# Kernel tuning notes

Hardware: AMD Instinct MI355X
Metric: run time of the kernel (lower is better)

Reference implementation:

```python
import jax, jax.numpy as jnp
import numpy as np
from jax import lax

PERM_AD = np.array([3, 0, 1, 6, 4, 2, 7, 8, 5])  # angular-difference kernel permutation
IDX_HD_POS = np.array([0, 3, 6]); IDX_HD_NEG = np.array([2, 5, 8])
IDX_VD_POS = np.array([0, 1, 2]); IDX_VD_NEG = np.array([6, 7, 8])
TOP_K = 1
THETA = 1.0


def conv2d_3x3(x, w, b):
    # x: [B,C,H,W], w: [O,I,3,3], b: [O]; stride 1, padding 1
    out = lax.conv_general_dilated(x, w, window_strides=(1, 1), padding=((1, 1), (1, 1)),
                                   dimension_numbers=('NCHW', 'OIHW', 'NCHW'))
    return out + b[None, :, None, None]


def setup_inputs() -> dict:
    key = jax.random.key(0)
    ks = jax.random.split(key, 12)
    B, C, H, W, E = 16, 64, 128, 128, 5

    def winit(k, shape, fan_in):
        return jax.random.normal(k, shape, jnp.float32) * (1.0 / np.sqrt(fan_in))

    return {
        'x': jax.random.normal(ks[0], (B, C, H, W), jnp.float32),
        'noise': jax.random.normal(ks[1], (B, E), jnp.float32),
        'w_gate': winit(ks[2], (C, E), C), 'b_gate': jnp.zeros((E,), jnp.float32),
        'w_noise': winit(ks[3], (C, E), C), 'b_noise': jnp.zeros((E,), jnp.float32),
        'w1': winit(ks[4], (C, C, 3, 3), C * 9), 'b1': jnp.zeros((C,), jnp.float32),
        'w_cd': winit(ks[5], (C, C, 3, 3), C * 9), 'b_cd': jnp.zeros((C,), jnp.float32),
        'w_hd': winit(ks[6], (C, C, 3), C * 3), 'b_hd': jnp.zeros((C,), jnp.float32),
        'w_vd': winit(ks[7], (C, C, 3), C * 3), 'b_vd': jnp.zeros((C,), jnp.float32),
        'w_ad': winit(ks[8], (C, C, 3, 3), C * 9), 'b_ad': jnp.zeros((C,), jnp.float32),
    }


def reference(x, noise, w_gate, b_gate, w_noise, b_noise,
              w1, b1, w_cd, b_cd, w_hd, b_hd, w_vd, b_vd, w_ad, b_ad):
    B, C, H, W = x.shape
    E = w_gate.shape[1]

    # ---- NoisyTopkRouter on globally pooled features ----
    pooled = x.mean(axis=(2, 3))                      # [B, C]
    logits = pooled @ w_gate + b_gate                 # [B, E]
    noise_logits = pooled @ w_noise + b_noise         # [B, E]
    noisy = logits + noise * jax.nn.softplus(noise_logits)
    topv, topi = lax.top_k(noisy, TOP_K)              # [B, k]
    sparse = jnp.full_like(noisy, -jnp.inf)
    sparse = sparse.at[jnp.arange(B)[:, None], topi].set(topv)
    gates = jax.nn.softmax(sparse, axis=-1)           # [B, E]; 0 for unselected, gate weight otherwise

    # ---- Difference-convolution expert kernels ----
    wcd_f = w_cd.reshape(C, C, 9)
    wcd = wcd_f.at[:, :, 4].add(-wcd_f.sum(-1)).reshape(C, C, 3, 3)   # center = w4 - sum(all)
    whd = jnp.zeros((C, C, 9), x.dtype).at[:, :, IDX_HD_POS].set(w_hd).at[:, :, IDX_HD_NEG].set(-w_hd).reshape(C, C, 3, 3)
    wvd = jnp.zeros((C, C, 9), x.dtype).at[:, :, IDX_VD_POS].set(w_vd).at[:, :, IDX_VD_NEG].set(-w_vd).reshape(C, C, 3, 3)
    wad_f = w_ad.reshape(C, C, 9)
    wad = (wad_f - THETA * wad_f[:, :, PERM_AD]).reshape(C, C, 3, 3)

    outs = jnp.stack([
        conv2d_3x3(x, w1, b1),
        conv2d_3x3(x, wcd, b_cd),
        conv2d_3x3(x, whd, b_hd),
        conv2d_3x3(x, wvd, b_vd),
        conv2d_3x3(x, wad, b_ad),
    ], axis=0)                                        # [E, B, C, H, W]

    # ---- SparseDispatcher.combine: per-example softmax over flattened depth, gate-weighted scatter-add ----
    flat = outs.reshape(E, B, C * H * W)
    sm = jax.nn.softmax(flat, axis=-1)                # softmax over depth dim, as in combine()
    combined = jnp.einsum('ebd,be->bd', sm, gates)    # gates are 0 for non-dispatched (expert,example) pairs
    return combined.reshape(B, C, H, W)
```

## Files before the change

### kernel.cpp

```cpp
#include <hip/hip_runtime.h>
#include <math.h>

#define B_  16
#define C_  64
#define E_  5

typedef __bf16  bf16x8 __attribute__((ext_vector_type(8)));
typedef float   f32x4  __attribute__((ext_vector_type(4)));

#define WS_WEFFB   0
#define WS_BIAS    368640
#define WS_POOL    369920
#define WS_Z       374016
#define WS_CNT     374080
#define WS_XT      376128
#define WS_EXP     33930560ull
#define WS_NEED_A  67484992ull

static __device__ __forceinline__ unsigned short f2bf(float f) {
    unsigned int u = __float_as_uint(f);
    unsigned int r = (u + 0x7fffu + ((u >> 16) & 1u)) >> 16;
    return (unsigned short)r;
}

__global__ __launch_bounds__(256) void transpose_build_kernel(
        const float* __restrict__ x, unsigned short* __restrict__ x_t,
        float* __restrict__ pooled,
        const float* __restrict__ w1, const float* __restrict__ w_cd,
        const float* __restrict__ w_hd, const float* __restrict__ w_vd,
        const float* __restrict__ w_ad,
        const float* __restrict__ b1, const float* __restrict__ b_cd,
        const float* __restrict__ b_hd, const float* __restrict__ b_vd,
        const float* __restrict__ b_ad,
        unsigned short* __restrict__ wEffB, float* __restrict__ biasEff) {
    int bid = blockIdx.x;
    int t = threadIdx.x;

    if (bid >= 2048) {
        int gid = (bid - 2048) * 256 + t;
        if (gid < E_ * 36864) {
            int e   = gid / 36864;
            int r   = gid % 36864;
            int g   = r / 18432;
            int r2  = r % 18432;
            int tap = r2 / 2048;
            int r3  = r2 % 2048;
            int q   = r3 / 512;
            int r4  = r3 % 512;
            int co  = r4 / 8;
            int j   = r4 % 8;
            int ci = g * 32 + q * 8 + j;
            int base9 = (co * 64 + ci) * 9;
            int base3 = (co * 64 + ci) * 3;
            float v = 0.f;
            if (e == 0) {
                v = w1[base9 + tap];
            } else if (e == 1) {
                if (tap == 4) {
                    float s = 0.f;
                    #pragma unroll
                    for (int k = 0; k < 9; k++) s += w_cd[base9 + k];
                    v = w_cd[base9 + 4] - s;
                } else {
                    v = w_cd[base9 + tap];
                }
            } else if (e == 2) {
                int m = tap % 3;
                if (m == 0) v = w_hd[base3 + tap / 3];
                else if (m == 2) v = -w_hd[base3 + tap / 3];
            } else if (e == 3) {
                if (tap < 3) v = w_vd[base3 + tap];
                else if (tap >= 6) v = -w_vd[base3 + tap - 6];
            } else {
                const int PERM[9] = {3, 0, 1, 6, 4, 2, 7, 8, 5};
                v = w_ad[base9 + tap] - w_ad[base9 + PERM[tap]];
            }
            wEffB[gid] = f2bf(v);
        } else if (gid < E_ * 36864 + E_ * 64) {
            int jj = gid - E_ * 36864;
            int e = jj / 64, co = jj % 64;
            const float* bs;
            switch (e) {
                case 0: bs = b1; break;
                case 1: bs = b_cd; break;
                case 2: bs = b_hd; break;
                case 3: bs = b_vd; break;
                default: bs = b_ad; break;
            }
            biasEff[jj] = bs[co];
        }
        return;
    }

    int b = bid >> 7, row = bid & 127;
    int wave = t >> 6, l = t & 63;
    int half = l >> 5;
    int c4 = l & 31;

    __shared__ unsigned short T[128][72];

    const float* xb = x + (size_t)b * (64 * 16384) + row * 128;

    #pragma unroll
    for (int it = 0; it < 8; it++) {
        int ci = wave * 16 + it * 2 + half;
        float4 v = *(const float4*)(xb + (size_t)ci * 16384 + c4 * 4);
        float p = v.x + v.y + v.z + v.w;
        p += __shfl_down(p, 16, 32);
        p += __shfl_down(p, 8, 32);
        p += __shfl_down(p, 4, 32);
        p += __shfl_down(p, 2, 32);
        p += __shfl_down(p, 1, 32);
        if (c4 == 0) atomicAdd(&pooled[b * 64 + ci], p * (1.0f / 16384.0f));
        int colb = c4 * 4;
        T[colb + 0][ci] = f2bf(v.x);
        T[colb + 1][ci] = f2bf(v.y);
        T[colb + 2][ci] = f2bf(v.z);
        T[colb + 3][ci] = f2bf(v.w);
    }
    __syncthreads();

    unsigned short* dst = x_t + ((size_t)(b * 128 + row) * 128) * 64;
    #pragma unroll
    for (int k = 0; k < 4; k++) {
        int chunk = t + k * 256;
        int col = chunk >> 3, c8 = chunk & 7;
        uint4 vv = *(const uint4*)&T[col][c8 * 8];
        *(uint4*)(dst + col * 64 + c8 * 8) = vv;
    }
}

__global__ __launch_bounds__(256, 4) void conv_mfma_kernel(
        const unsigned short* __restrict__ x_t, const unsigned short* __restrict__ wEffB,
        const float* __restrict__ biasEff,
        const float* __restrict__ pooled, const float* __restrict__ noise,
        const float* __restrict__ w_gate, const float* __restrict__ b_gate,
        const float* __restrict__ w_noise, const float* __restrict__ b_noise,
        unsigned short* __restrict__ expw, float* __restrict__ outf,
        float* __restrict__ Z, int direct_f32) {
    int bid = blockIdx.x;
    int b = bid >> 6;
    int rem = bid & 63;
    int rg = rem >> 1;
    int ch = rem & 1;

    int t = threadIdx.x;
    int wave = t >> 6;
    int lane = t & 63;
    int ln = lane & 15;
    int q = lane >> 4;

    __shared__ __align__(16) unsigned short A_lds[3 * 4 * 66 * 8];
    __shared__ __align__(16) unsigned short Xs[4 * 4 * 68 * 8];
    __shared__ float zs[4];
    __shared__ int   se_sh;

    if (wave == 0) {
        float pv = pooled[b * C_ + lane];
        float ge[E_], ne[E_];
        #pragma unroll
        for (int e = 0; e < E_; e++) {
            ge[e] = pv * w_gate[lane * E_ + e];
            ne[e] = pv * w_noise[lane * E_ + e];
        }
        #pragma unroll
        for (int off = 32; off; off >>= 1) {
            #pragma unroll
            for (int e = 0; e < E_; e++) {
                ge[e] += __shfl_xor(ge[e], off, 64);
                ne[e] += __shfl_xor(ne[e], off, 64);
            }
        }
        if (lane == 0) {
            float best = -1e30f; int bi = 0;
            #pragma unroll
            for (int e = 0; e < E_; e++) {
                float lg = ge[e] + b_gate[e];
                float nz = ne[e] + b_noise[e];
                float sp = log1pf(expf(nz));
                float v = lg + noise[b * E_ + e] * sp;
                if (v > best) { best = v; bi = e; }
            }
            se_sh = bi;
        }
    }
    __syncthreads();
    int e = se_sh;

    f32x4 acc[4][4];
    #pragma unroll
    for (int i = 0; i < 4; i++)
        #pragma unroll
        for (int jn = 0; jn < 4; jn++)
            acc[i][jn] = (f32x4){0.f, 0.f, 0.f, 0.f};

    const unsigned short* xb = x_t + (size_t)b * (128 * 128 * 64);
    const unsigned short* we = wEffB + (size_t)e * 36864;

    for (int g = 0; g < 2; g++) {
        const uint4* asrc = (const uint4*)(we + g * 18432);
        #pragma unroll
        for (int chunk = 0; chunk < 3; chunk++) {
            if (chunk == 0) {
                for (int j = t; j < 1056; j += 256) {
                    int xr = j / 264;
                    int r2 = j % 264;
                    int col = r2 >> 2;
                    int qq = r2 & 3;
                    int irow = rg * 4 - 1 + xr;
                    int icol = ch * 64 - 1 + col;
                    uint4 v = make_uint4(0, 0, 0, 0);
                    if ((unsigned)irow < 128u && (unsigned)icol < 128u)
                        v = *(const uint4*)(xb + ((size_t)irow * 128 + icol) * 64 + g * 32 + qq * 8);
                    *(uint4*)&Xs[(((xr & 3) * 4 + qq) * 68 + col) * 8] = v;
                }
            } else {
                int xr = 3 + chunk;
                int irow = rg * 4 - 1 + xr;
                for (int j = t; j < 264; j += 256) {
                    int col = j >> 2;
                    int qq = j & 3;
                    int icol = ch * 64 - 1 + col;
                    uint4 v = make_uint4(0, 0, 0, 0);
                    if ((unsigned)irow < 128u && (unsigned)icol < 128u)
                        v = *(const uint4*)(xb + ((size_t)irow * 128 + icol) * 64 + g * 32 + qq * 8);
                    *(uint4*)&Xs[(((xr & 3) * 4 + qq) * 68 + col) * 8] = v;
                }
            }
            #pragma unroll
            for (int k = 0; k < 3; k++) {
                int j = t + k * 256;
                int slotrow = j >> 6;
                int m = j & 63;
                *(uint4*)&A_lds[(slotrow * 66 + m) * 8] = asrc[chunk * 768 + j];
            }
            __syncthreads();

            int xrl = wave + chunk;
            #pragma unroll
            for (int tl = 0; tl < 3; tl++) {
                bf16x8 af[4], bfr[4];
                #pragma unroll
                for (int mt = 0; mt < 4; mt++)
                    af[mt] = *(const bf16x8*)&A_lds[((tl * 4 + q) * 66 + mt * 16 + ln) * 8];
                #pragma unroll
                for (int t4 = 0; t4 < 4; t4++)
                    bfr[t4] = *(const bf16x8*)&Xs[(((xrl & 3) * 4 + q) * 68 + t4 * 16 + ln + tl) * 8];
                #pragma unroll
                for (int mt = 0; mt < 4; mt++)
                    #pragma unroll
                    for (int t4 = 0; t4 < 4; t4++)
                        acc[mt][t4] = __builtin_amdgcn_mfma_f32_16x16x32_bf16(
                            af[mt], bfr[t4], acc[mt][t4], 0, 0, 0);
            }
            __syncthreads();
        }
    }

    int orow = rg * 4 + wave;
    float bsum = 0.f;
    size_t obase = (size_t)b * (64 * 16384);
    #pragma unroll
    for (int mt = 0; mt < 4; mt++) {
        float4 bias4 = *(const float4*)(biasEff + e * 64 + mt * 16 + q * 4);
        const float* bp = (const float*)&bias4;
        #pragma unroll
        for (int r = 0; r < 4; r++) {
            int co = mt * 16 + q * 4 + r;
            size_t cb = obase + (size_t)co * 16384 + (size_t)orow * 128;
            #pragma unroll
            for (int t4 = 0; t4 < 4; t4++) {
                float ev = __expf(acc[mt][t4][r] + bp[r]);
                bsum += ev;
                int ocol = ch * 64 + t4 * 16 + ln;
                if (direct_f32) outf[cb + ocol] = ev;
                else            expw[cb + ocol] = f2bf(ev);
            }
        }
    }
    for (int off = 32; off; off >>= 1) bsum += __shfl_down(bsum, off, 64);
    if (lane == 0) zs[wave] = bsum;
    __syncthreads();
    if (t == 0) atomicAdd(&Z[b], zs[0] + zs[1] + zs[2] + zs[3]);
}

#define N_UINT4 2097152
__global__ __launch_bounds__(256) void scale_bf16_kernel(
        const unsigned short* __restrict__ expw, const float* __restrict__ Z,
        float* __restrict__ out) {
    __shared__ float sinv[B_];
    if (threadIdx.x < B_) sinv[threadIdx.x] = 1.0f / Z[threadIdx.x];
    __syncthreads();
    for (int gid = blockIdx.x * 256 + threadIdx.x; gid < N_UINT4; gid += 2048 * 256) {
        int b = gid >> 17;
        float s = sinv[b];
        uint4 r = ((const uint4*)expw)[gid];
        f32x4 o0, o1;
        o0[0] = __uint_as_float(r.x << 16) * s;
        o0[1] = __uint_as_float(r.x & 0xffff0000u) * s;
        o0[2] = __uint_as_float(r.y << 16) * s;
        o0[3] = __uint_as_float(r.y & 0xffff0000u) * s;
        o1[0] = __uint_as_float(r.z << 16) * s;
        o1[1] = __uint_as_float(r.z & 0xffff0000u) * s;
        o1[2] = __uint_as_float(r.w << 16) * s;
        o1[3] = __uint_as_float(r.w & 0xffff0000u) * s;
        __builtin_nontemporal_store(o0, &((f32x4*)out)[gid * 2]);
        __builtin_nontemporal_store(o1, &((f32x4*)out)[gid * 2 + 1]);
    }
}

#define N_FLOAT4 4194304
__global__ __launch_bounds__(256) void scale_inplace_kernel(
        float* __restrict__ out, const float* __restrict__ Z) {
    __shared__ float sinv[B_];
    if (threadIdx.x < B_) sinv[threadIdx.x] = 1.0f / Z[threadIdx.x];
    __syncthreads();
    for (int gid = blockIdx.x * 256 + threadIdx.x; gid < N_FLOAT4; gid += 2048 * 256) {
        int b = gid >> 18;
        float s = sinv[b];
        float4 v = ((float4*)out)[gid];
        v.x *= s; v.y *= s; v.z *= s; v.w *= s;
        ((float4*)out)[gid] = v;
    }
}

extern "C" void kernel_launch(void* const* d_in, const int* in_sizes, int n_in,
                              void* d_out, int out_size, void* d_ws, size_t ws_size,
                              hipStream_t stream) {
    const float* x       = (const float*)d_in[0];
    const float* noise   = (const float*)d_in[1];
    const float* w_gate  = (const float*)d_in[2];
    const float* b_gate  = (const float*)d_in[3];
    const float* w_noise = (const float*)d_in[4];
    const float* b_noise = (const float*)d_in[5];
    const float* w1      = (const float*)d_in[6];
    const float* b1      = (const float*)d_in[7];
    const float* w_cd    = (const float*)d_in[8];
    const float* b_cd    = (const float*)d_in[9];
    const float* w_hd    = (const float*)d_in[10];
    const float* b_hd    = (const float*)d_in[11];
    const float* w_vd    = (const float*)d_in[12];
    const float* b_vd    = (const float*)d_in[13];
    const float* w_ad    = (const float*)d_in[14];
    const float* b_ad    = (const float*)d_in[15];

    char* ws = (char*)d_ws;
    unsigned short* wEffB   = (unsigned short*)(ws + WS_WEFFB);
    float*          biasEff = (float*)(ws + WS_BIAS);
    float*          pooled  = (float*)(ws + WS_POOL);
    float*          Zbuf    = (float*)(ws + WS_Z);
    unsigned short* x_t     = (unsigned short*)(ws + WS_XT);
    unsigned short* expw    = (unsigned short*)(ws + WS_EXP);

    float* out = (float*)d_out;
    int mode_a = (ws_size >= WS_NEED_A) ? 1 : 0;

    hipMemsetAsync(pooled, 0, 4160, stream);

    transpose_build_kernel<<<2048 + 722, 256, 0, stream>>>(
        x, x_t, pooled, w1, w_cd, w_hd, w_vd, w_ad,
        b1, b_cd, b_hd, b_vd, b_ad, wEffB, biasEff);

    conv_mfma_kernel<<<1024, 256, 0, stream>>>(
        x_t, wEffB, biasEff, pooled, noise, w_gate, b_gate, w_noise, b_noise,
        expw, out, Zbuf, mode_a ? 0 : 1);

    if (mode_a)
        scale_bf16_kernel<<<2048, 256, 0, stream>>>(expw, Zbuf, out);
    else
        scale_inplace_kernel<<<2048, 256, 0, stream>>>(out, Zbuf);
}
```

Measured before the change: 221.3 us.

## Register-prefetch weight chunks, stage all six input rows at once, raise MFMA priority

The conv kernel now loads all six halo input rows into a larger LDS buffer once per channel group, instead of refilling a ring of four rows per chunk. The next weight chunk is prefetched into registers while the MFMAs for the current chunk run, so global weight loads overlap compute. s_setprio raises wave priority around the MFMA loop. The bf16 scale kernel switches to nontemporal loads. The larger LDS footprint may reduce occupancy, and the extra prefetch registers add register pressure.

```diff
diff --git a/kernel.cpp b/kernel.cpp
--- a/kernel.cpp
+++ b/kernel.cpp
@@ -7,6 +7,7 @@
 
 typedef __bf16  bf16x8 __attribute__((ext_vector_type(8)));
 typedef float   f32x4  __attribute__((ext_vector_type(4)));
+typedef unsigned int u32x4 __attribute__((ext_vector_type(4)));
 
 #define WS_WEFFB   0
 #define WS_BIAS    368640
@@ -151,7 +152,7 @@
     int q = lane >> 4;
 
     __shared__ __align__(16) unsigned short A_lds[3 * 4 * 66 * 8];
-    __shared__ __align__(16) unsigned short Xs[4 * 4 * 68 * 8];
+    __shared__ __align__(16) unsigned short Xs[6 * 4 * 68 * 8];
     __shared__ float zs[4];
     __shared__ int   se_sh;
 
@@ -196,47 +197,43 @@
 
     const unsigned short* xb = x_t + (size_t)b * (128 * 128 * 64);
     const unsigned short* we = wEffB + (size_t)e * 36864;
+    const uint4* asrc0 = (const uint4*)we;
+    const uint4* asrc1 = (const uint4*)(we + 18432);
+
+    int awrow = t >> 6, awm = t & 63;
+
+    uint4 a0 = asrc0[t], a1 = asrc0[t + 256], a2 = asrc0[t + 512];
 
     for (int g = 0; g < 2; g++) {
-        const uint4* asrc = (const uint4*)(we + g * 18432);
+        for (int j = t; j < 1584; j += 256) {
+            int xr = j / 264;
+            int r2 = j % 264;
+            int col = r2 >> 2;
+            int qq = r2 & 3;
+            int irow = rg * 4 - 1 + xr;
+            int icol = ch * 64 - 1 + col;
+            uint4 v = make_uint4(0, 0, 0, 0);
+            if ((unsigned)irow < 128u && (unsigned)icol < 128u)
+                v = *(const uint4*)(xb + ((size_t)irow * 128 + icol) * 64 + g * 32 + qq * 8);
+            *(uint4*)&Xs[((xr * 4 + qq) * 68 + col) * 8] = v;
+        }
+
         #pragma unroll
         for (int chunk = 0; chunk < 3; chunk++) {
-            if (chunk == 0) {
-                for (int j = t; j < 1056; j += 256) {
-                    int xr = j / 264;
-                    int r2 = j % 264;
-                    int col = r2 >> 2;
-                    int qq = r2 & 3;
-                    int irow = rg * 4 - 1 + xr;
-                    int icol = ch * 64 - 1 + col;
-                    uint4 v = make_uint4(0, 0, 0, 0);
-                    if ((unsigned)irow < 128u && (unsigned)icol < 128u)
-                        v = *(const uint4*)(xb + ((size_t)irow * 128 + icol) * 64 + g * 32 + qq * 8);
-                    *(uint4*)&Xs[(((xr & 3) * 4 + qq) * 68 + col) * 8] = v;
-                }
-            } else {
-                int xr = 3 + chunk;
-                int irow = rg * 4 - 1 + xr;
-                for (int j = t; j < 264; j += 256) {
-                    int col = j >> 2;
-                    int qq = j & 3;
-                    int icol = ch * 64 - 1 + col;
-                    uint4 v = make_uint4(0, 0, 0, 0);
-                    if ((unsigned)irow < 128u && (unsigned)icol < 128u)
-                        v = *(const uint4*)(xb + ((size_t)irow * 128 + icol) * 64 + g * 32 + qq * 8);
-                    *(uint4*)&Xs[(((xr & 3) * 4 + qq) * 68 + col) * 8] = v;
-                }
-            }
-            #pragma unroll
-            for (int k = 0; k < 3; k++) {
-                int j = t + k * 256;
-                int slotrow = j >> 6;
-                int m = j & 63;
-                *(uint4*)&A_lds[(slotrow * 66 + m) * 8] = asrc[chunk * 768 + j];
-            }
+            *(uint4*)&A_lds[((awrow     ) * 66 + awm) * 8] = a0;
+            *(uint4*)&A_lds[((awrow +  4) * 66 + awm) * 8] = a1;
+            *(uint4*)&A_lds[((awrow +  8) * 66 + awm) * 8] = a2;
             __syncthreads();
 
-            int xrl = wave + chunk;
+            int nc = g * 3 + chunk + 1;
+            if (nc < 6) {
+                const uint4* an = (nc < 3) ? (asrc0 + nc * 768)
+                                           : (asrc1 + (nc - 3) * 768);
+                a0 = an[t]; a1 = an[t + 256]; a2 = an[t + 512];
+            }
+
+            int xr = wave + chunk;
+            __builtin_amdgcn_s_setprio(1);
             #pragma unroll
             for (int tl = 0; tl < 3; tl++) {
                 bf16x8 af[4], bfr[4];
@@ -245,7 +242,7 @@
                     af[mt] = *(const bf16x8*)&A_lds[((tl * 4 + q) * 66 + mt * 16 + ln) * 8];
                 #pragma unroll
                 for (int t4 = 0; t4 < 4; t4++)
-                    bfr[t4] = *(const bf16x8*)&Xs[(((xrl & 3) * 4 + q) * 68 + t4 * 16 + ln + tl) * 8];
+                    bfr[t4] = *(const bf16x8*)&Xs[((xr * 4 + q) * 68 + t4 * 16 + ln + tl) * 8];
                 #pragma unroll
                 for (int mt = 0; mt < 4; mt++)
                     #pragma unroll
@@ -253,6 +250,7 @@
                         acc[mt][t4] = __builtin_amdgcn_mfma_f32_16x16x32_bf16(
                             af[mt], bfr[t4], acc[mt][t4], 0, 0, 0);
             }
+            __builtin_amdgcn_s_setprio(0);
             __syncthreads();
         }
     }
@@ -294,16 +292,16 @@
     for (int gid = blockIdx.x * 256 + threadIdx.x; gid < N_UINT4; gid += 2048 * 256) {
         int b = gid >> 17;
         float s = sinv[b];
-        uint4 r = ((const uint4*)expw)[gid];
+        u32x4 r = __builtin_nontemporal_load(&((const u32x4*)expw)[gid]);
         f32x4 o0, o1;
-        o0[0] = __uint_as_float(r.x << 16) * s;
-        o0[1] = __uint_as_float(r.x & 0xffff0000u) * s;
-        o0[2] = __uint_as_float(r.y << 16) * s;
-        o0[3] = __uint_as_float(r.y & 0xffff0000u) * s;
-        o1[0] = __uint_as_float(r.z << 16) * s;
-        o1[1] = __uint_as_float(r.z & 0xffff0000u) * s;
-        o1[2] = __uint_as_float(r.w << 16) * s;
-        o1[3] = __uint_as_float(r.w & 0xffff0000u) * s;
+        o0[0] = __uint_as_float(r[0] << 16) * s;
+        o0[1] = __uint_as_float(r[0] & 0xffff0000u) * s;
+        o0[2] = __uint_as_float(r[1] << 16) * s;
+        o0[3] = __uint_as_float(r[1] & 0xffff0000u) * s;
+        o1[0] = __uint_as_float(r[2] << 16) * s;
+        o1[1] = __uint_as_float(r[2] & 0xffff0000u) * s;
+        o1[2] = __uint_as_float(r[3] << 16) * s;
+        o1[3] = __uint_as_float(r[3] & 0xffff0000u) * s;
         __builtin_nontemporal_store(o0, &((f32x4*)out)[gid * 2]);
         __builtin_nontemporal_store(o1, &((f32x4*)out)[gid * 2 + 1]);
     }
```

After: 224.8 us. Within noise of the previous version (+1.6%).
